# Kernel tuning notes

Measured on AMD Instinct MI355X. Metric: run time of the kernel, lower is better.

Reference implementation:

```python
import jax, jax.numpy as jnp
import numpy as np

B, T, C = 2, 2048, 1024
NH = 16

def setup_inputs() -> dict:
    key = jax.random.key(0)
    ks = jax.random.split(key, 5)
    s = 0.02
    return {
        "x": jax.random.normal(ks[0], (B, T, C), dtype=jnp.float32),
        "w_attn": jax.random.normal(ks[1], (C, 3 * C), dtype=jnp.float32) * s,
        "b_attn": jax.random.normal(ks[2], (3 * C,), dtype=jnp.float32) * s,
        "w_proj": jax.random.normal(ks[3], (C, C), dtype=jnp.float32) * s,
        "b_proj": jax.random.normal(ks[4], (C,), dtype=jnp.float32) * s,
        "n_heads": NH,
    }

def reference(x, w_attn, b_attn, w_proj, b_proj, n_heads):
    Bx, Tx, Cx = x.shape
    hd = Cx // n_heads
    qkv = x @ w_attn + b_attn                      # [B,T,3C]
    q, k, v = jnp.split(qkv, 3, axis=-1)
    # [B,T,H,hd] -> [B,H,T,hd]
    q = q.reshape(Bx, Tx, n_heads, hd).transpose(0, 2, 1, 3)
    k = k.reshape(Bx, Tx, n_heads, hd).transpose(0, 2, 1, 3)
    v = v.reshape(Bx, Tx, n_heads, hd).transpose(0, 2, 1, 3)
    scale = 1.0 / np.sqrt(hd).astype(np.float32)
    att = jnp.einsum('bhqd,bhkd->bhqk', q, k) * scale   # [B,H,T,T]
    causal = jnp.tril(jnp.ones((Tx, Tx), dtype=bool))
    att = jnp.where(causal[None, None], att, -jnp.inf)
    att = jax.nn.softmax(att, axis=-1)
    y = jnp.einsum('bhqk,bhkd->bhqd', att, v)            # [B,H,T,hd]
    y = y.transpose(0, 2, 1, 3).reshape(Bx, Tx, Cx)
    return y @ w_proj + b_proj
```

## Files before the change

### kernel.cpp

```cpp
#include <hip/hip_runtime.h>

typedef __bf16 bf16x8 __attribute__((ext_vector_type(8)));
typedef __bf16 bf16x4 __attribute__((ext_vector_type(4)));
typedef float  f32x4  __attribute__((ext_vector_type(4)));
typedef float  f32x16 __attribute__((ext_vector_type(16)));
typedef unsigned int u32;

#define MFMA_BF16(a, b, c) __builtin_amdgcn_mfma_f32_16x16x32_bf16((a), (b), (c), 0, 0, 0)
#define MFMA32(a, b, c) __builtin_amdgcn_mfma_f32_32x32x16_bf16((a), (b), (c), 0, 0, 0)
#define NEG_INF (-1e30f)
#define SCL 0.18033688f

__device__ __forceinline__ void gld16(const void* g, void* l) {
  __builtin_amdgcn_global_load_lds(
      (const __attribute__((address_space(1))) void*)g,
      (__attribute__((address_space(3))) void*)l, 16, 0, 0);
}

__global__ __launch_bounds__(256) void prep(
    const float* __restrict__ x, __bf16* __restrict__ xb,
    const float* __restrict__ wa, __bf16* __restrict__ wta,
    const float* __restrict__ wp, __bf16* __restrict__ wtp) {
  __shared__ float t[32][33];
  const int tid = threadIdx.x;
  const int bx = blockIdx.x;
  if (bx < 2048) {
    int i = (bx * 256 + tid) * 8;
    float4 a = *(const float4*)&x[i];
    float4 b = *(const float4*)&x[i + 4];
    bf16x8 v;
    v[0] = (__bf16)a.x; v[1] = (__bf16)a.y; v[2] = (__bf16)a.z; v[3] = (__bf16)a.w;
    v[4] = (__bf16)b.x; v[5] = (__bf16)b.y; v[6] = (__bf16)b.z; v[7] = (__bf16)b.w;
    *(bf16x8*)&xb[i] = v;
    return;
  }
  const float* in; __bf16* out; int R, C, bxx, byy;
  if (bx < 5120) { in = wa; out = wta; R = 1024; C = 3072;
                   bxx = (bx - 2048) % 96; byy = (bx - 2048) / 96; }
  else           { in = wp; out = wtp; R = 1024; C = 1024;
                   bxx = (bx - 5120) % 32; byy = (bx - 5120) / 32; }
  int tx = tid & 31, ty = tid >> 5;
  int xx = bxx * 32 + tx, y0 = byy * 32 + ty;
#pragma unroll
  for (int i = 0; i < 4; ++i)
    t[ty + 8 * i][tx] = in[(size_t)(y0 + 8 * i) * C + xx];
  __syncthreads();
  int x2 = byy * 32 + tx;
#pragma unroll
  for (int i = 0; i < 4; ++i)
    out[(size_t)(bxx * 32 + ty + 8 * i) * R + x2] = (__bf16)t[tx][ty + 8 * i];
}

#define BN 128
#define BK 64

template <int BMT, typename TC>
__global__ __launch_bounds__(256) void gemm_bt_bias(
    const __bf16* __restrict__ A, const __bf16* __restrict__ Bt,
    const float* __restrict__ bias, TC* __restrict__ Cmat,
    int M, int N, int K) {
  constexpr int NI = BMT / 32;
  __shared__ __align__(16) __bf16 As[BMT * BK];
  __shared__ __align__(16) __bf16 Bs[BN * BK];
  int tid = threadIdx.x;
  int wave = tid >> 6, lane = tid & 63;
  int l16 = lane & 15, quad = lane >> 4;
  int wm = wave >> 1, wn = wave & 1;
  int m0 = blockIdx.y * BMT, n0 = blockIdx.x * BN;

  f32x4 acc[NI][4];
#pragma unroll
  for (int i = 0; i < NI; ++i)
#pragma unroll
    for (int j = 0; j < 4; ++j) acc[i][j] = (f32x4){0.f, 0.f, 0.f, 0.f};

  int row = tid >> 3;
  int kc = ((tid & 7) ^ ((tid >> 3) & 7)) * 8;
  int xr = (l16 & 7) * 8;

  for (int k0 = 0; k0 < K; k0 += BK) {
#pragma unroll
    for (int i = 0; i < NI; ++i)
      gld16(&A[(size_t)(m0 + row + i * 32) * K + k0 + kc],
            (char*)As + (i * 256 + wave * 64) * 16);
#pragma unroll
    for (int j = 0; j < 4; ++j)
      gld16(&Bt[(size_t)(n0 + row + j * 32) * K + k0 + kc],
            (char*)Bs + (j * 256 + wave * 64) * 16);
    __syncthreads();
#pragma unroll
    for (int ks = 0; ks < 2; ++ks) {
      bf16x8 af[NI], bfr[4];
#pragma unroll
      for (int i = 0; i < NI; ++i)
        af[i] = *(const bf16x8*)&As[(wm * (BMT / 2) + i * 16 + l16) * BK +
                                    ((ks * 32 + quad * 8) ^ xr)];
#pragma unroll
      for (int j = 0; j < 4; ++j)
        bfr[j] = *(const bf16x8*)&Bs[(wn * 64 + j * 16 + l16) * BK +
                                     ((ks * 32 + quad * 8) ^ xr)];
#pragma unroll
      for (int i = 0; i < NI; ++i)
#pragma unroll
        for (int j = 0; j < 4; ++j) acc[i][j] = MFMA_BF16(af[i], bfr[j], acc[i][j]);
    }
    __syncthreads();
  }
#pragma unroll
  for (int i = 0; i < NI; ++i) {
#pragma unroll
    for (int j = 0; j < 4; ++j) {
      int col = n0 + wn * 64 + j * 16 + l16;
      float bv = bias[col];
#pragma unroll
      for (int r = 0; r < 4; ++r) {
        int rw = m0 + wm * (BMT / 2) + i * 16 + quad * 4 + r;
        Cmat[(size_t)rw * N + col] = (TC)(acc[i][j][r] + bv);
      }
    }
  }
}

#define BARX do { asm volatile("" ::: "memory"); __builtin_amdgcn_s_barrier(); \
                  asm volatile("" ::: "memory"); } while (0)
#define WLGKM do { asm volatile("s_waitcnt lgkmcnt(0)" ::: "memory"); \
                   __builtin_amdgcn_sched_barrier(0); } while (0)
#define WVM8 asm volatile("s_waitcnt vmcnt(8)" ::: "memory")
#define STA8(SBUF, SKS, T) do { \
    gld16(srcA1 + (size_t)(T) * 64 + (SKS) * 32, (char*)&As[SBUF][SKS][0] + tid * 16); \
    gld16(srcA2 + (size_t)(T) * 64 + (SKS) * 32, (char*)&As[SBUF][SKS][0] + tid * 16 + 8192); \
  } while (0)
#define STB8(SBUF, SKS, T) do { \
    gld16(srcB1 + (size_t)(T) * 64 + (SKS) * 32, (char*)&Bs[SBUF][SKS][0] + tid * 16); \
    gld16(srcB2 + (size_t)(T) * 64 + (SKS) * 32, (char*)&Bs[SBUF][SKS][0] + tid * 16 + 8192); \
  } while (0)
#define LDA8(CBUF, CKS) do { \
    const __bf16* p0_ = &As[CBUF][CKS][(wm * 128 + l16) * 32 + xrd]; \
    af[0] = *(const bf16x8*)(p0_);        af[1] = *(const bf16x8*)(p0_ + 512); \
    af[2] = *(const bf16x8*)(p0_ + 1024); af[3] = *(const bf16x8*)(p0_ + 1536); \
    const __bf16* p1_ = p0_ + 2048; \
    af[4] = *(const bf16x8*)(p1_);        af[5] = *(const bf16x8*)(p1_ + 512); \
    af[6] = *(const bf16x8*)(p1_ + 1024); af[7] = *(const bf16x8*)(p1_ + 1536); \
  } while (0)
#define LDB3(CBUF, CKS) do { \
    const __bf16* p_ = &Bs[CBUF][CKS][(wn * 48 + l16) * 32 + xrd]; \
    bfr[0] = *(const bf16x8*)(p_);       bfr[1] = *(const bf16x8*)(p_ + 512); \
    bfr[2] = *(const bf16x8*)(p_ + 1024); \
  } while (0)
#define MM24 do { \
    __builtin_amdgcn_s_setprio(1); \
    _Pragma("unroll") for (int mi_ = 0; mi_ < 8; ++mi_) \
    _Pragma("unroll") for (int nj_ = 0; nj_ < 3; ++nj_) \
      acc[mi_][nj_] = MFMA_BF16(af[mi_], bfr[nj_], acc[mi_][nj_]); \
    __builtin_amdgcn_s_setprio(0); \
  } while (0)

__global__ __launch_bounds__(512, 2) void gemm_qkv_8ph(
    const __bf16* __restrict__ A, const __bf16* __restrict__ Bt,
    const float* __restrict__ bias, __bf16* __restrict__ qkv,
    __bf16* __restrict__ vt) {
  constexpr int GK = 1024, GN = 3072, NT = 16;
  __shared__ __align__(16) __bf16 As[2][2][256 * 32];
  __shared__ __align__(16) __bf16 Bs[2][2][256 * 32];
  const int tid = threadIdx.x;
  const int wave = tid >> 6, lane = tid & 63;
  const int l16 = lane & 15, quad = lane >> 4;
  const int wm = wave >> 2, wn = wave & 3;
  const int m0 = blockIdx.y * 256, n0 = blockIdx.x * 192;

  const int row0 = tid >> 2;
  const int kc = (((tid & 3) ^ ((row0 >> 1) & 3)) * 8);
  const int xrd = (quad ^ ((l16 >> 1) & 3)) * 8;

  const __bf16* srcA1 = A + (size_t)(m0 + row0) * GK + kc;
  const __bf16* srcA2 = srcA1 + (size_t)128 * GK;
  const __bf16* srcB1 = Bt + (size_t)(n0 + row0) * GK + kc;
  const int br2 = (row0 + 128 < 192) ? row0 + 128 : 191;
  const __bf16* srcB2 = Bt + (size_t)(n0 + br2) * GK + kc;

  f32x4 acc[8][3];
#pragma unroll
  for (int m = 0; m < 8; ++m)
#pragma unroll
    for (int n = 0; n < 3; ++n) acc[m][n] = (f32x4){0.f, 0.f, 0.f, 0.f};

  STA8(0, 0, 0); STB8(0, 0, 0);
  STA8(0, 1, 0); STB8(0, 1, 0);
  STA8(1, 0, 1); STB8(1, 0, 1);
  WVM8;
  BARX;

  bf16x8 af[8], bfr[3];
#pragma unroll 1
  for (int i = 0; i < NT / 2; ++i) {
    const int v = 2 * i + 1;
    const int t2 = (2 * i + 2 < NT) ? 2 * i + 2 : NT - 1;
    const int t3 = (2 * i + 3 < NT) ? 2 * i + 3 : NT - 1;
    LDA8(0, 0); LDB3(0, 0); STA8(1, 1, v); STB8(1, 1, v);
    BARX; WLGKM; MM24; WVM8; BARX;
    LDA8(0, 1); LDB3(0, 1); STA8(0, 0, t2); STB8(0, 0, t2);
    BARX; WLGKM; MM24; WVM8; BARX;
    LDA8(1, 0); LDB3(1, 0); STA8(0, 1, t2); STB8(0, 1, t2);
    BARX; WLGKM; MM24; WVM8; BARX;
    LDA8(1, 1); LDB3(1, 1); STA8(1, 0, t3); STB8(1, 0, t3);
    BARX; WLGKM; MM24; WVM8; BARX;
  }

#pragma unroll
  for (int n = 0; n < 3; ++n) {
    const int c0 = n0 + wn * 48 + n * 16;
    const int col = c0 + l16;
    const float bv = bias[col];
    if (c0 < 2048) {
#pragma unroll
      for (int m = 0; m < 8; ++m) {
        const int rw = m0 + wm * 128 + m * 16 + quad * 4;
#pragma unroll
        for (int r = 0; r < 4; ++r)
          qkv[(size_t)(rw + r) * GN + col] = (__bf16)(acc[m][n][r] + bv);
      }
    } else {
      const int h = (col - 2048) >> 6, d = col & 63;
#pragma unroll
      for (int m = 0; m < 8; ++m) {
        const int t0 = m0 + wm * 128 + m * 16 + quad * 4;
        const int b = t0 >> 11, tt = t0 & 2047;
        bf16x4 pb;
#pragma unroll
        for (int r = 0; r < 4; ++r) pb[r] = (__bf16)(acc[m][n][r] + bv);
        *(bf16x4*)&vt[(size_t)((b * 16 + h) * 64 + d) * 2048 + tt] = pb;
      }
    }
  }
}

#define CVTPK(D, LO, HI) \
  asm("v_cvt_pk_bf16_f32 %0, %1, %2" : "=v"(D) : "v"(LO), "v"(HI))
#define SWAP32(DST, SRC) \
  asm("v_permlane32_swap_b32 %0, %1" : "+v"(DST), "+v"(SRC))

__device__ __forceinline__ bf16x8 mk8(u32 a, u32 b, u32 c, u32 d) {
  union { u32 u[4]; bf16x8 h; } x;
  x.u[0] = a; x.u[1] = b; x.u[2] = c; x.u[3] = d;
  return x.h;
}

__global__ __launch_bounds__(512, 4) void attn_causal(
    const __bf16* __restrict__ qkv, const __bf16* __restrict__ vt,
    __bf16* __restrict__ y) {
  __shared__ __align__(16) __bf16 smem[2][2][2][64 * 64];
  const int tid = threadIdx.x;
  const int wave = tid >> 6, lane = tid & 63;
  const int l32 = lane & 31, hi = lane >> 5;
  const int qh = wave >> 1, kh = wave & 1;
  const int bh = blockIdx.x;
  const int b = bh >> 4, h = bh & 15;
  const int RS = 3072;
  const int by = (int)blockIdx.y;
  const int qb = (by < 8) ? 15 - by : by - 8;
  const int nit = qb + 1;
  const int ktmax = 2 * qb + (qh >> 1);

  const int row8 = tid >> 3;
  const int kcs = (((tid & 7) ^ (row8 & 7) ^ ((row8 >> 3) & 3)) * 8);
  const __bf16* kbase = qkv + (size_t)(b * 2048) * RS + 1024 + h * 64 + kcs;
  const __bf16* vbase = vt + (size_t)(bh * 64) * 2048 + kcs;
  const int xr = (l32 & 7) ^ ((l32 >> 3) & 3);

  const __bf16* qp = qkv +
      (size_t)(b * 2048 + qb * 128 + qh * 32 + l32) * RS + h * 64 + hi * 8;
  bf16x8 qf[4];
#pragma unroll
  for (int kc = 0; kc < 4; ++kc) qf[kc] = *(const bf16x8*)(qp + kc * 16);

  float l4[4] = {0.f, 0.f, 0.f, 0.f};
  f32x16 o0, o1;
#pragma unroll
  for (int r = 0; r < 16; ++r) { o0[r] = 0.f; o1[r] = 0.f; }

#pragma unroll
  for (int s = 0; s < 2; ++s) {
    gld16(kbase + (size_t)(s * 64 + row8) * RS, (char*)smem[0][0][s] + tid * 16);
    gld16(vbase + (size_t)row8 * 2048 + s * 64, (char*)smem[1][0][s] + tid * 16);
  }
  __syncthreads();

  for (int it = 0; it < nit; ++it) {
    const int cur = it & 1;
    if (it < qb) {
      const int kb2 = (it + 1) * 128;
#pragma unroll
      for (int s = 0; s < 2; ++s) {
        gld16(kbase + (size_t)(kb2 + s * 64 + row8) * RS,
              (char*)smem[0][cur ^ 1][s] + tid * 16);
        gld16(vbase + (size_t)row8 * 2048 + kb2 + s * 64,
              (char*)smem[1][cur ^ 1][s] + tid * 16);
      }
    }

    const int kt = 2 * it + kh;
    if (kt <= ktmax) {
      const __bf16* Kc = smem[0][cur][kh];
      const __bf16* Vc = smem[1][cur][kh];

      f32x16 c0, c1;
#pragma unroll
      for (int r = 0; r < 16; ++r) { c0[r] = 0.f; c1[r] = 0.f; }
      __builtin_amdgcn_s_setprio(1);
#pragma unroll
      for (int kc = 0; kc < 4; ++kc) {
        const int sw = ((kc * 2 + hi) ^ xr) << 3;
        bf16x8 kf0 = *(const bf16x8*)&Kc[l32 * 64 + sw];
        bf16x8 kf1 = *(const bf16x8*)&Kc[(32 + l32) * 64 + sw];
        c0 = MFMA32(kf0, qf[kc], c0);
        c1 = MFMA32(kf1, qf[kc], c1);
      }
      __builtin_amdgcn_s_setprio(0);

      if (kt == ktmax) {
        const int qloc = qh * 32 + l32 - (kt - 2 * qb) * 64;
#pragma unroll
        for (int r = 0; r < 16; ++r) {
          const int kl = (r & 3) + 8 * (r >> 2) + 4 * hi;
          if (kl > qloc) c0[r] = NEG_INF;
          if (32 + kl > qloc) c1[r] = NEG_INF;
        }
      }

      bf16x8 pb[4];
#pragma unroll
      for (int kb = 0; kb < 2; ++kb) {
        float pv[16];
#pragma unroll
        for (int r = 0; r < 16; ++r) {
          const float sv = (kb ? c1[r] : c0[r]);
          pv[r] = __builtin_amdgcn_exp2f(sv * SCL);
          l4[r & 3] += pv[r];
        }
        u32 a0, a1, b0, b1;
        CVTPK(a0, pv[0], pv[1]);   CVTPK(a1, pv[2], pv[3]);
        CVTPK(b0, pv[4], pv[5]);   CVTPK(b1, pv[6], pv[7]);
        SWAP32(a0, b0); SWAP32(a1, b1);
        pb[kb * 2 + 0] = mk8(a0, a1, b0, b1);
        CVTPK(a0, pv[8], pv[9]);   CVTPK(a1, pv[10], pv[11]);
        CVTPK(b0, pv[12], pv[13]); CVTPK(b1, pv[14], pv[15]);
        SWAP32(a0, b0); SWAP32(a1, b1);
        pb[kb * 2 + 1] = mk8(a0, a1, b0, b1);

        __builtin_amdgcn_s_setprio(1);
#pragma unroll
        for (int kq = 0; kq < 2; ++kq) {
          const int kc = kb * 2 + kq;
          const int sw = ((kc * 2 + hi) ^ xr) << 3;
          bf16x8 vf0 = *(const bf16x8*)&Vc[l32 * 64 + sw];
          bf16x8 vf1 = *(const bf16x8*)&Vc[(32 + l32) * 64 + sw];
          o0 = MFMA32(vf0, pb[kc], o0);
          o1 = MFMA32(vf1, pb[kc], o1);
        }
        __builtin_amdgcn_s_setprio(0);
      }
    }
    __syncthreads();
  }

  float lred = (l4[0] + l4[1]) + (l4[2] + l4[3]);
  lred += __shfl_xor(lred, 32);

  float* sc = (float*)smem;
  if (kh == 1) {
    float* ob = sc + qh * 2048;
#pragma unroll
    for (int r = 0; r < 16; ++r) {
      ob[r * 64 + lane] = o0[r];
      ob[1024 + r * 64 + lane] = o1[r];
    }
    if (lane < 32) sc[8192 + qh * 32 + lane] = lred;
  }
  __syncthreads();
  if (kh == 0) {
    const float* ob = sc + qh * 2048;
    lred += sc[8192 + qh * 32 + l32];
    const float inv = 1.f / lred;
    const int orow = b * 2048 + qb * 128 + qh * 32 + l32;
    __bf16* yb = y + (size_t)orow * 1024 + h * 64 + hi * 4;
#pragma unroll
    for (int db = 0; db < 2; ++db) {
#pragma unroll
      for (int g = 0; g < 4; ++g) {
        bf16x4 w;
#pragma unroll
        for (int j = 0; j < 4; ++j) {
          const float v = (db ? o1[g * 4 + j] : o0[g * 4 + j]) +
                          ob[db * 1024 + (g * 4 + j) * 64 + lane];
          w[j] = (__bf16)(v * inv);
        }
        *(bf16x4*)&yb[db * 32 + g * 8] = w;
      }
    }
  }
}

extern "C" void kernel_launch(void* const* d_in, const int* in_sizes, int n_in,
                              void* d_out, int out_size, void* d_ws, size_t ws_size,
                              hipStream_t stream) {
  (void)in_sizes; (void)n_in; (void)out_size; (void)ws_size;
  const float* x      = (const float*)d_in[0];
  const float* w_attn = (const float*)d_in[1];
  const float* b_attn = (const float*)d_in[2];
  const float* w_proj = (const float*)d_in[3];
  const float* b_proj = (const float*)d_in[4];
  float* out = (float*)d_out;

  __bf16* wt_attn = (__bf16*)d_ws;
  __bf16* wt_proj = wt_attn + (size_t)3072 * 1024;
  __bf16* qkv     = wt_proj + (size_t)1024 * 1024;
  __bf16* ybuf    = qkv + (size_t)4096 * 3072;
  __bf16* vtbuf   = ybuf + (size_t)4096 * 1024;

  prep<<<6144, 256, 0, stream>>>(x, ybuf, w_attn, wt_attn, w_proj, wt_proj);

  gemm_qkv_8ph<<<dim3(3072 / 192, 4096 / 256), 512, 0, stream>>>(
      ybuf, wt_attn, b_attn, qkv, vtbuf);

  attn_causal<<<dim3(32, 16), 512, 0, stream>>>(qkv, vtbuf, ybuf);

  gemm_bt_bias<64, float><<<dim3(1024 / BN, 4096 / 64), 256, 0, stream>>>(
      ybuf, wt_proj, b_proj, out, 4096, 1024, 1024);
}
```

Measured before the change: 170.6 us.

## Halve QKV GEMM M-tile to 128 rows to double grid and occupancy

Shrinks the QKV projection tile from 256x192 to 128x192. The grid doubles to 512 blocks, which fills the 256 CUs more evenly. Loads of the B tile are now split by wave so the waits are per wave (vmcnt 6 or 4), and the launch bound is raised to 4 blocks per CU. The aim is to cut wave-quantization tail and raise occupancy, at the cost of less reuse of each B tile per block and more global traffic for B.

```diff
diff --git a/kernel.cpp b/kernel.cpp
--- a/kernel.cpp
+++ b/kernel.cpp
@@ -125,85 +125,81 @@
                   asm volatile("" ::: "memory"); } while (0)
 #define WLGKM do { asm volatile("s_waitcnt lgkmcnt(0)" ::: "memory"); \
                    __builtin_amdgcn_sched_barrier(0); } while (0)
-#define WVM8 asm volatile("s_waitcnt vmcnt(8)" ::: "memory")
-#define STA8(SBUF, SKS, T) do { \
-    gld16(srcA1 + (size_t)(T) * 64 + (SKS) * 32, (char*)&As[SBUF][SKS][0] + tid * 16); \
-    gld16(srcA2 + (size_t)(T) * 64 + (SKS) * 32, (char*)&As[SBUF][SKS][0] + tid * 16 + 8192); \
+#define WVMC do { if (wave < 4) asm volatile("s_waitcnt vmcnt(6)" ::: "memory"); \
+                  else          asm volatile("s_waitcnt vmcnt(4)" ::: "memory"); } while (0)
+#define STA(SBUF, SKS, T) \
+    gld16(srcA1 + (size_t)(T) * 64 + (SKS) * 32, (char*)&As[SBUF][SKS][0] + tid * 16)
+#define STB(SBUF, SKS, T) do { \
+    gld16(srcB1 + (size_t)(T) * 64 + (SKS) * 32, (char*)&Bs[SBUF][SKS][0] + tid * 16); \
+    if (wave < 4) \
+      gld16(srcB2 + (size_t)(T) * 64 + (SKS) * 32, \
+            (char*)&Bs[SBUF][SKS][0] + 8192 + tid * 16); \
   } while (0)
-#define STB8(SBUF, SKS, T) do { \
-    gld16(srcB1 + (size_t)(T) * 64 + (SKS) * 32, (char*)&Bs[SBUF][SKS][0] + tid * 16); \
-    gld16(srcB2 + (size_t)(T) * 64 + (SKS) * 32, (char*)&Bs[SBUF][SKS][0] + tid * 16 + 8192); \
-  } while (0)
-#define LDA8(CBUF, CKS) do { \
-    const __bf16* p0_ = &As[CBUF][CKS][(wm * 128 + l16) * 32 + xrd]; \
-    af[0] = *(const bf16x8*)(p0_);        af[1] = *(const bf16x8*)(p0_ + 512); \
-    af[2] = *(const bf16x8*)(p0_ + 1024); af[3] = *(const bf16x8*)(p0_ + 1536); \
-    const __bf16* p1_ = p0_ + 2048; \
-    af[4] = *(const bf16x8*)(p1_);        af[5] = *(const bf16x8*)(p1_ + 512); \
-    af[6] = *(const bf16x8*)(p1_ + 1024); af[7] = *(const bf16x8*)(p1_ + 1536); \
+#define LDA4(CBUF, CKS) do { \
+    const __bf16* p_ = &As[CBUF][CKS][(wm * 64 + l16) * 32 + xrd]; \
+    af[0] = *(const bf16x8*)(p_);        af[1] = *(const bf16x8*)(p_ + 512); \
+    af[2] = *(const bf16x8*)(p_ + 1024); af[3] = *(const bf16x8*)(p_ + 1536); \
   } while (0)
 #define LDB3(CBUF, CKS) do { \
     const __bf16* p_ = &Bs[CBUF][CKS][(wn * 48 + l16) * 32 + xrd]; \
     bfr[0] = *(const bf16x8*)(p_);       bfr[1] = *(const bf16x8*)(p_ + 512); \
     bfr[2] = *(const bf16x8*)(p_ + 1024); \
   } while (0)
-#define MM24 do { \
+#define MM12 do { \
     __builtin_amdgcn_s_setprio(1); \
-    _Pragma("unroll") for (int mi_ = 0; mi_ < 8; ++mi_) \
+    _Pragma("unroll") for (int mi_ = 0; mi_ < 4; ++mi_) \
     _Pragma("unroll") for (int nj_ = 0; nj_ < 3; ++nj_) \
       acc[mi_][nj_] = MFMA_BF16(af[mi_], bfr[nj_], acc[mi_][nj_]); \
     __builtin_amdgcn_s_setprio(0); \
   } while (0)
 
-__global__ __launch_bounds__(512, 2) void gemm_qkv_8ph(
+__global__ __launch_bounds__(512, 4) void gemm_qkv_8ph(
     const __bf16* __restrict__ A, const __bf16* __restrict__ Bt,
     const float* __restrict__ bias, __bf16* __restrict__ qkv,
     __bf16* __restrict__ vt) {
   constexpr int GK = 1024, GN = 3072, NT = 16;
-  __shared__ __align__(16) __bf16 As[2][2][256 * 32];
-  __shared__ __align__(16) __bf16 Bs[2][2][256 * 32];
+  __shared__ __align__(16) __bf16 As[2][2][128 * 32];
+  __shared__ __align__(16) __bf16 Bs[2][2][192 * 32];
   const int tid = threadIdx.x;
   const int wave = tid >> 6, lane = tid & 63;
   const int l16 = lane & 15, quad = lane >> 4;
   const int wm = wave >> 2, wn = wave & 3;
-  const int m0 = blockIdx.y * 256, n0 = blockIdx.x * 192;
+  const int m0 = blockIdx.y * 128, n0 = blockIdx.x * 192;
 
   const int row0 = tid >> 2;
   const int kc = (((tid & 3) ^ ((row0 >> 1) & 3)) * 8);
   const int xrd = (quad ^ ((l16 >> 1) & 3)) * 8;
 
   const __bf16* srcA1 = A + (size_t)(m0 + row0) * GK + kc;
-  const __bf16* srcA2 = srcA1 + (size_t)128 * GK;
   const __bf16* srcB1 = Bt + (size_t)(n0 + row0) * GK + kc;
-  const int br2 = (row0 + 128 < 192) ? row0 + 128 : 191;
-  const __bf16* srcB2 = Bt + (size_t)(n0 + br2) * GK + kc;
-
-  f32x4 acc[8][3];
-#pragma unroll
-  for (int m = 0; m < 8; ++m)
+  const __bf16* srcB2 = Bt + (size_t)(n0 + 128 + (row0 & 63)) * GK + kc;
+
+  f32x4 acc[4][3];
+#pragma unroll
+  for (int m = 0; m < 4; ++m)
 #pragma unroll
     for (int n = 0; n < 3; ++n) acc[m][n] = (f32x4){0.f, 0.f, 0.f, 0.f};
 
-  STA8(0, 0, 0); STB8(0, 0, 0);
-  STA8(0, 1, 0); STB8(0, 1, 0);
-  STA8(1, 0, 1); STB8(1, 0, 1);
-  WVM8;
+  STA(0, 0, 0); STB(0, 0, 0);
+  STA(0, 1, 0); STB(0, 1, 0);
+  STA(1, 0, 1); STB(1, 0, 1);
+  WVMC;
   BARX;
 
-  bf16x8 af[8], bfr[3];
+  bf16x8 af[4], bfr[3];
 #pragma unroll 1
   for (int i = 0; i < NT / 2; ++i) {
     const int v = 2 * i + 1;
     const int t2 = (2 * i + 2 < NT) ? 2 * i + 2 : NT - 1;
     const int t3 = (2 * i + 3 < NT) ? 2 * i + 3 : NT - 1;
-    LDA8(0, 0); LDB3(0, 0); STA8(1, 1, v); STB8(1, 1, v);
-    BARX; WLGKM; MM24; WVM8; BARX;
-    LDA8(0, 1); LDB3(0, 1); STA8(0, 0, t2); STB8(0, 0, t2);
-    BARX; WLGKM; MM24; WVM8; BARX;
-    LDA8(1, 0); LDB3(1, 0); STA8(0, 1, t2); STB8(0, 1, t2);
-    BARX; WLGKM; MM24; WVM8; BARX;
-    LDA8(1, 1); LDB3(1, 1); STA8(1, 0, t3); STB8(1, 0, t3);
-    BARX; WLGKM; MM24; WVM8; BARX;
+    LDA4(0, 0); LDB3(0, 0); STA(1, 1, v); STB(1, 1, v);
+    BARX; WLGKM; MM12; WVMC; BARX;
+    LDA4(0, 1); LDB3(0, 1); STA(0, 0, t2); STB(0, 0, t2);
+    BARX; WLGKM; MM12; WVMC; BARX;
+    LDA4(1, 0); LDB3(1, 0); STA(0, 1, t2); STB(0, 1, t2);
+    BARX; WLGKM; MM12; WVMC; BARX;
+    LDA4(1, 1); LDB3(1, 1); STA(1, 0, t3); STB(1, 0, t3);
+    BARX; WLGKM; MM12; WVMC; BARX;
   }
 
 #pragma unroll
@@ -213,8 +209,8 @@
     const float bv = bias[col];
     if (c0 < 2048) {
 #pragma unroll
-      for (int m = 0; m < 8; ++m) {
-        const int rw = m0 + wm * 128 + m * 16 + quad * 4;
+      for (int m = 0; m < 4; ++m) {
+        const int rw = m0 + wm * 64 + m * 16 + quad * 4;
 #pragma unroll
         for (int r = 0; r < 4; ++r)
           qkv[(size_t)(rw + r) * GN + col] = (__bf16)(acc[m][n][r] + bv);
@@ -222,8 +218,8 @@
     } else {
       const int h = (col - 2048) >> 6, d = col & 63;
 #pragma unroll
-      for (int m = 0; m < 8; ++m) {
-        const int t0 = m0 + wm * 128 + m * 16 + quad * 4;
+      for (int m = 0; m < 4; ++m) {
+        const int t0 = m0 + wm * 64 + m * 16 + quad * 4;
         const int b = t0 >> 11, tt = t0 & 2047;
         bf16x4 pb;
 #pragma unroll
@@ -419,7 +415,7 @@
 
   prep<<<6144, 256, 0, stream>>>(x, ybuf, w_attn, wt_attn, w_proj, wt_proj);
 
-  gemm_qkv_8ph<<<dim3(3072 / 192, 4096 / 256), 512, 0, stream>>>(
+  gemm_qkv_8ph<<<dim3(3072 / 192, 4096 / 128), 512, 0, stream>>>(
       ybuf, wt_attn, b_attn, qkv, vtbuf);
 
   attn_causal<<<dim3(32, 16), 512, 0, stream>>>(qkv, vtbuf, ybuf);
```

Result: no change. 169.5 us (-0.6%).
